# Performance work log

Measured on AMD Instinct MI355X. Metric: run time of the kernel, lower is better.

Reference implementation:

```python
import jax, jax.numpy as jnp
import numpy as np

N = 65536
SIZES = [3, 256, 256, 256, 256, 1]
NU = np.float32(0.01 / np.pi)  # viscosity coefficient 0.01/pi


def setup_inputs() -> dict:
    key = jax.random.key(0)
    ks = jax.random.split(key, 16)
    inp = {
        "t": jax.random.uniform(ks[0], (N, 1), dtype=jnp.float32),
        "x": jax.random.uniform(ks[1], (N, 1), dtype=jnp.float32),
        "y": jax.random.uniform(ks[2], (N, 1), dtype=jnp.float32),
    }
    for i in range(len(SIZES) - 1):
        fan_in, fan_out = SIZES[i], SIZES[i + 1]
        scale = jnp.float32(1.0 / np.sqrt(fan_in))
        inp[f"W{i}"] = jax.random.normal(ks[3 + i], (fan_in, fan_out), dtype=jnp.float32) * scale
        inp[f"b{i}"] = jnp.zeros((fan_out,), dtype=jnp.float32)
    return inp


def reference(t, x, y, W0, b0, W1, b1, W2, b2, W3, b3, W4, b4):
    Ws = (W0, W1, W2, W3, W4)
    bs = (b0, b1, b2, b3, b4)

    def u_scalar(pt):  # pt: (3,) -> scalar u(t,x,y)
        h = pt
        for W, b in zip(Ws[:-1], bs[:-1]):
            h = jnp.tanh(h @ W + b)
        return (h @ Ws[-1] + bs[-1])[0]

    def point(pt):
        u, g = jax.value_and_grad(u_scalar)(pt)          # g = (u_t, u_x, u_y)
        H = jax.jacfwd(jax.grad(u_scalar))(pt)           # 3x3 Hessian (fwd-over-rev)
        f = g[0] + u * g[1] + u * g[2] - NU * (H[1, 1] + H[2, 2])
        return u, f

    pts = jnp.concatenate((t, x, y), axis=1)  # [N, 3]
    u, f = jax.vmap(point)(pts)
    return u[:, None], f[:, None]
```

## Files before the change

### kernel.cpp

```cpp
#include <hip/hip_runtime.h>

#define NPTS 65536
#define NU_F 0.0031830988618379067f

typedef __attribute__((ext_vector_type(8))) _Float16 half8v;
typedef __attribute__((ext_vector_type(2))) __fp16   fp16x2;
typedef __attribute__((ext_vector_type(4))) float    f32x4;

__device__ __forceinline__ unsigned pk2(float a, float b) {
    union { fp16x2 h; unsigned u; } c;
    c.h = __builtin_amdgcn_cvt_pkrtz(a, b);
    return c.u;
}

__device__ __forceinline__ void jet5(float z, float zt, float zx, float zy, float zl,
                                     float& s0, float& s1, float& s2, float& s3, float& s4) {
    float e  = __expf(2.0f * z);
    float a  = 1.0f - 2.0f * __builtin_amdgcn_rcpf(e + 1.0f);
    float ap = 1.0f - a * a;
    s0 = a;
    s1 = ap * zt;
    s2 = ap * zx;
    s3 = ap * zy;
    float q = zx * zx + zy * zy;
    s4 = ap * __builtin_fmaf(-2.0f * a, q, zl);
}

__device__ __forceinline__ int swzoff(int sp, int byteInRow) {
    return (sp << 9) + (byteInRow ^ ((sp & 31) << 4));
}
__device__ __forceinline__ void storeJ2(char* baseB, int sp, int j0,
                                        unsigned lo, unsigned hi) {
    *(uint2*)(baseB + swzoff(sp, j0 * 2)) = make_uint2(lo, hi);
}

__global__ __launch_bounds__(256)
void pinn_prep_kernel(const float* __restrict__ W1, const float* __restrict__ W2,
                      const float* __restrict__ W3, _Float16* __restrict__ ws) {
    int gid  = blockIdx.x * 256 + threadIdx.x;
    int l    = gid >> 13;
    int rem  = gid & 8191;
    int M    = rem >> 9;
    int kt   = (rem >> 6) & 7;
    int lane = rem & 63;
    const float* W = (l == 0) ? W1 : (l == 1) ? W2 : W3;
    int j  = M * 16 + (lane & 15);
    int k0 = kt * 32 + (lane >> 4) * 8;
    union { _Float16 h[8]; half8v v; } hf;
    #pragma unroll
    for (int jj = 0; jj < 8; ++jj)
        hf.h[jj] = (_Float16)W[(k0 + jj) * 256 + j];
    ((half8v*)ws)[l * 8192 + (M * 8 + kt) * 64 + lane] = hf.v;
}

__global__ __launch_bounds__(512, 2)
void pinn_burger2d_kernel(
    const float* __restrict__ t, const float* __restrict__ x, const float* __restrict__ y,
    const float* __restrict__ W0, const float* __restrict__ b0,
    const float* __restrict__ b1, const float* __restrict__ b2, const float* __restrict__ b3,
    const float* __restrict__ W4, const float* __restrict__ b4,
    const _Float16* __restrict__ wf, float* __restrict__ out)
{
    __shared__ _Float16 BjS[5 * 16 * 256];
    char* bjB = (char*)BjS;

    const int tid  = threadIdx.x;
    const int lane = tid & 63;
    const int wv   = tid >> 6;
    const int p    = lane & 15;
    const int quad = lane >> 4;
    const int base = blockIdx.x * 16;
    const int gi   = base + p;

    const float tv = t[gi], xv = x[gi], yv = y[gi];

    #pragma unroll
    for (int m = 0; m < 2; ++m) {
        const int j0 = wv * 32 + m * 16 + quad * 4;
        float4 w0t = *(const float4*)(W0 + j0);
        float4 w0x = *(const float4*)(W0 + 256 + j0);
        float4 w0y = *(const float4*)(W0 + 512 + j0);
        float4 bb  = *(const float4*)(b0 + j0);
        float wtA[4] = {w0t.x, w0t.y, w0t.z, w0t.w};
        float wxA[4] = {w0x.x, w0x.y, w0x.z, w0x.w};
        float wyA[4] = {w0y.x, w0y.y, w0y.z, w0y.w};
        float bbA[4] = {bb.x, bb.y, bb.z, bb.w};
        float ss[5][4];
        #pragma unroll
        for (int i = 0; i < 4; ++i) {
            float z = tv * wtA[i] + xv * wxA[i] + yv * wyA[i] + bbA[i];
            jet5(z, wtA[i], wxA[i], wyA[i], 0.0f,
                 ss[0][i], ss[1][i], ss[2][i], ss[3][i], ss[4][i]);
        }
        #pragma unroll
        for (int s = 0; s < 5; ++s)
            storeJ2(bjB, s * 16 + p, j0, pk2(ss[s][0], ss[s][1]), pk2(ss[s][2], ss[s][3]));
    }
    __syncthreads();

    f32x4 acc[2][5];

    for (int li = 0; li < 3; ++li) {
        #pragma unroll
        for (int m = 0; m < 2; ++m)
            #pragma unroll
            for (int c = 0; c < 5; ++c)
                acc[m][c] = (f32x4)(0.0f);

        const half8v* whf = (const half8v*)wf + li * 8192;

        #pragma unroll 2
        for (int kt = 0; kt < 8; ++kt) {
            const int bRow = kt * 64 + quad * 16;
            half8v bv0 = *(const half8v*)(bjB + swzoff(     p, bRow));
            half8v bv1 = *(const half8v*)(bjB + swzoff(16 + p, bRow));
            half8v bv2 = *(const half8v*)(bjB + swzoff(32 + p, bRow));
            half8v bv3 = *(const half8v*)(bjB + swzoff(48 + p, bRow));
            half8v bv4 = *(const half8v*)(bjB + swzoff(64 + p, bRow));
            __builtin_amdgcn_s_setprio(1);
            #pragma unroll
            for (int m = 0; m < 2; ++m) {
                half8v wh = whf[((wv * 2 + m) * 8 + kt) * 64 + lane];
                acc[m][0] = __builtin_amdgcn_mfma_f32_16x16x32_f16(wh, bv0, acc[m][0], 0, 0, 0);
                acc[m][1] = __builtin_amdgcn_mfma_f32_16x16x32_f16(wh, bv1, acc[m][1], 0, 0, 0);
                acc[m][2] = __builtin_amdgcn_mfma_f32_16x16x32_f16(wh, bv2, acc[m][2], 0, 0, 0);
                acc[m][3] = __builtin_amdgcn_mfma_f32_16x16x32_f16(wh, bv3, acc[m][3], 0, 0, 0);
                acc[m][4] = __builtin_amdgcn_mfma_f32_16x16x32_f16(wh, bv4, acc[m][4], 0, 0, 0);
            }
            __builtin_amdgcn_s_setprio(0);
        }
        __syncthreads();

        if (li < 2) {
            const float* bL = (li == 0) ? b1 : b2;
            #pragma unroll
            for (int m = 0; m < 2; ++m) {
                const int j0 = (wv * 2 + m) * 16 + quad * 4;
                float4 bb = *(const float4*)(bL + j0);
                float bbA[4] = {bb.x, bb.y, bb.z, bb.w};
                float ss[5][4];
                #pragma unroll
                for (int i = 0; i < 4; ++i) {
                    jet5(acc[m][0][i] + bbA[i], acc[m][1][i], acc[m][2][i],
                         acc[m][3][i], acc[m][4][i],
                         ss[0][i], ss[1][i], ss[2][i], ss[3][i], ss[4][i]);
                }
                #pragma unroll
                for (int s = 0; s < 5; ++s)
                    storeJ2(bjB, s * 16 + p, j0, pk2(ss[s][0], ss[s][1]), pk2(ss[s][2], ss[s][3]));
            }
            __syncthreads();
        }
    }

    float part[5] = {0, 0, 0, 0, 0};
    #pragma unroll
    for (int m = 0; m < 2; ++m) {
        const int j0 = (wv * 2 + m) * 16 + quad * 4;
        float4 bb = *(const float4*)(b3 + j0);
        float4 w4 = *(const float4*)(W4 + j0);
        float bbA[4] = {bb.x, bb.y, bb.z, bb.w};
        float w4A[4] = {w4.x, w4.y, w4.z, w4.w};
        #pragma unroll
        for (int i = 0; i < 4; ++i) {
            float s0, s1, s2, s3, s4;
            jet5(acc[m][0][i] + bbA[i], acc[m][1][i], acc[m][2][i],
                 acc[m][3][i], acc[m][4][i], s0, s1, s2, s3, s4);
            part[0] += s0 * w4A[i];
            part[1] += s1 * w4A[i];
            part[2] += s2 * w4A[i];
            part[3] += s3 * w4A[i];
            part[4] += s4 * w4A[i];
        }
    }
    #pragma unroll
    for (int s = 0; s < 5; ++s) {
        part[s] += __shfl_xor(part[s], 16, 64);
        part[s] += __shfl_xor(part[s], 32, 64);
    }

    float* resf = (float*)BjS;
    if (lane < 16) {
        #pragma unroll
        for (int s = 0; s < 5; ++s) resf[(wv * 5 + s) * 16 + p] = part[s];
    }
    __syncthreads();

    if (tid < 16) {
        const int pp = tid;
        const int g  = base + pp;
        float u = b4[0], ut = 0, ux = 0, uy = 0, lap = 0;
        #pragma unroll
        for (int w = 0; w < 8; ++w) {
            u   += resf[(w * 5 + 0) * 16 + pp];
            ut  += resf[(w * 5 + 1) * 16 + pp];
            ux  += resf[(w * 5 + 2) * 16 + pp];
            uy  += resf[(w * 5 + 3) * 16 + pp];
            lap += resf[(w * 5 + 4) * 16 + pp];
        }
        out[g]        = u;
        out[NPTS + g] = ut + u * ux + u * uy - NU_F * lap;
    }
}

extern "C" void kernel_launch(void* const* d_in, const int* in_sizes, int n_in,
                              void* d_out, int out_size, void* d_ws, size_t ws_size,
                              hipStream_t stream) {
    const float* t  = (const float*)d_in[0];
    const float* x  = (const float*)d_in[1];
    const float* y  = (const float*)d_in[2];
    const float* W0 = (const float*)d_in[3];
    const float* b0 = (const float*)d_in[4];
    const float* W1 = (const float*)d_in[5];
    const float* b1 = (const float*)d_in[6];
    const float* W2 = (const float*)d_in[7];
    const float* b2 = (const float*)d_in[8];
    const float* W3 = (const float*)d_in[9];
    const float* b3 = (const float*)d_in[10];
    const float* W4 = (const float*)d_in[11];
    const float* b4 = (const float*)d_in[12];
    float* out = (float*)d_out;

    pinn_prep_kernel<<<96, 256, 0, stream>>>(W1, W2, W3, (_Float16*)d_ws);
    pinn_burger2d_kernel<<<NPTS / 16, 512, 0, stream>>>(
        t, x, y, W0, b0, b1, b2, b3, W4, b4, (const _Float16*)d_ws, out);
}
```

Before: 146.9 us.

## Process two 16-point tiles per block to reuse weight fragments

Each block now handles 32 points as two 16-point tiles with separate LDS activation buffers and accumulator sets. Each weight fragment loaded from global memory feeds MFMAs for both tiles, halving weight traffic per point and doubling independent MFMA chains. In exchange, accumulator registers and LDS per block double (80 KB), which may lower occupancy under the 2-block launch bound and cause spills.

```diff
diff --git a/kernel.cpp b/kernel.cpp
--- a/kernel.cpp
+++ b/kernel.cpp
@@ -61,18 +61,21 @@
     const float* __restrict__ W4, const float* __restrict__ b4,
     const _Float16* __restrict__ wf, float* __restrict__ out)
 {
-    __shared__ _Float16 BjS[5 * 16 * 256];
-    char* bjB = (char*)BjS;
+    __shared__ _Float16 BjS[2][5 * 16 * 256];
+    char* bufA = (char*)BjS[0];
+    char* bufB = (char*)BjS[1];
 
     const int tid  = threadIdx.x;
     const int lane = tid & 63;
     const int wv   = tid >> 6;
     const int p    = lane & 15;
     const int quad = lane >> 4;
-    const int base = blockIdx.x * 16;
-    const int gi   = base + p;
-
-    const float tv = t[gi], xv = x[gi], yv = y[gi];
+    const int base = blockIdx.x * 32;
+    const int giA  = base + p;
+    const int giB  = base + 16 + p;
+
+    const float tvA = t[giA], xvA = x[giA], yvA = y[giA];
+    const float tvB = t[giB], xvB = x[giB], yvB = y[giB];
 
     #pragma unroll
     for (int m = 0; m < 2; ++m) {
@@ -85,49 +88,80 @@
         float wxA[4] = {w0x.x, w0x.y, w0x.z, w0x.w};
         float wyA[4] = {w0y.x, w0y.y, w0y.z, w0y.w};
         float bbA[4] = {bb.x, bb.y, bb.z, bb.w};
-        float ss[5][4];
+        float sA[5][4], sB[5][4];
         #pragma unroll
         for (int i = 0; i < 4; ++i) {
-            float z = tv * wtA[i] + xv * wxA[i] + yv * wyA[i] + bbA[i];
-            jet5(z, wtA[i], wxA[i], wyA[i], 0.0f,
-                 ss[0][i], ss[1][i], ss[2][i], ss[3][i], ss[4][i]);
-        }
-        #pragma unroll
-        for (int s = 0; s < 5; ++s)
-            storeJ2(bjB, s * 16 + p, j0, pk2(ss[s][0], ss[s][1]), pk2(ss[s][2], ss[s][3]));
+            float zA = tvA * wtA[i] + xvA * wxA[i] + yvA * wyA[i] + bbA[i];
+            jet5(zA, wtA[i], wxA[i], wyA[i], 0.0f,
+                 sA[0][i], sA[1][i], sA[2][i], sA[3][i], sA[4][i]);
+            float zB = tvB * wtA[i] + xvB * wxA[i] + yvB * wyA[i] + bbA[i];
+            jet5(zB, wtA[i], wxA[i], wyA[i], 0.0f,
+                 sB[0][i], sB[1][i], sB[2][i], sB[3][i], sB[4][i]);
+        }
+        #pragma unroll
+        for (int s = 0; s < 5; ++s) {
+            storeJ2(bufA, s * 16 + p, j0, pk2(sA[s][0], sA[s][1]), pk2(sA[s][2], sA[s][3]));
+            storeJ2(bufB, s * 16 + p, j0, pk2(sB[s][0], sB[s][1]), pk2(sB[s][2], sB[s][3]));
+        }
     }
     __syncthreads();
 
-    f32x4 acc[2][5];
+    f32x4 accA[2][5], accB[2][5];
 
     for (int li = 0; li < 3; ++li) {
         #pragma unroll
         for (int m = 0; m < 2; ++m)
             #pragma unroll
-            for (int c = 0; c < 5; ++c)
-                acc[m][c] = (f32x4)(0.0f);
+            for (int c = 0; c < 5; ++c) {
+                accA[m][c] = (f32x4)(0.0f);
+                accB[m][c] = (f32x4)(0.0f);
+            }
 
         const half8v* whf = (const half8v*)wf + li * 8192;
 
         #pragma unroll 2
         for (int kt = 0; kt < 8; ++kt) {
             const int bRow = kt * 64 + quad * 16;
-            half8v bv0 = *(const half8v*)(bjB + swzoff(     p, bRow));
-            half8v bv1 = *(const half8v*)(bjB + swzoff(16 + p, bRow));
-            half8v bv2 = *(const half8v*)(bjB + swzoff(32 + p, bRow));
-            half8v bv3 = *(const half8v*)(bjB + swzoff(48 + p, bRow));
-            half8v bv4 = *(const half8v*)(bjB + swzoff(64 + p, bRow));
-            __builtin_amdgcn_s_setprio(1);
-            #pragma unroll
-            for (int m = 0; m < 2; ++m) {
-                half8v wh = whf[((wv * 2 + m) * 8 + kt) * 64 + lane];
-                acc[m][0] = __builtin_amdgcn_mfma_f32_16x16x32_f16(wh, bv0, acc[m][0], 0, 0, 0);
-                acc[m][1] = __builtin_amdgcn_mfma_f32_16x16x32_f16(wh, bv1, acc[m][1], 0, 0, 0);
-                acc[m][2] = __builtin_amdgcn_mfma_f32_16x16x32_f16(wh, bv2, acc[m][2], 0, 0, 0);
-                acc[m][3] = __builtin_amdgcn_mfma_f32_16x16x32_f16(wh, bv3, acc[m][3], 0, 0, 0);
-                acc[m][4] = __builtin_amdgcn_mfma_f32_16x16x32_f16(wh, bv4, acc[m][4], 0, 0, 0);
-            }
-            __builtin_amdgcn_s_setprio(0);
+            half8v wh0 = whf[((wv * 2 + 0) * 8 + kt) * 64 + lane];
+            half8v wh1 = whf[((wv * 2 + 1) * 8 + kt) * 64 + lane];
+            {
+                half8v v0 = *(const half8v*)(bufA + swzoff(     p, bRow));
+                half8v v1 = *(const half8v*)(bufA + swzoff(16 + p, bRow));
+                half8v v2 = *(const half8v*)(bufA + swzoff(32 + p, bRow));
+                half8v v3 = *(const half8v*)(bufA + swzoff(48 + p, bRow));
+                half8v v4 = *(const half8v*)(bufA + swzoff(64 + p, bRow));
+                __builtin_amdgcn_s_setprio(1);
+                accA[0][0] = __builtin_amdgcn_mfma_f32_16x16x32_f16(wh0, v0, accA[0][0], 0, 0, 0);
+                accA[0][1] = __builtin_amdgcn_mfma_f32_16x16x32_f16(wh0, v1, accA[0][1], 0, 0, 0);
+                accA[0][2] = __builtin_amdgcn_mfma_f32_16x16x32_f16(wh0, v2, accA[0][2], 0, 0, 0);
+                accA[0][3] = __builtin_amdgcn_mfma_f32_16x16x32_f16(wh0, v3, accA[0][3], 0, 0, 0);
+                accA[0][4] = __builtin_amdgcn_mfma_f32_16x16x32_f16(wh0, v4, accA[0][4], 0, 0, 0);
+                accA[1][0] = __builtin_amdgcn_mfma_f32_16x16x32_f16(wh1, v0, accA[1][0], 0, 0, 0);
+                accA[1][1] = __builtin_amdgcn_mfma_f32_16x16x32_f16(wh1, v1, accA[1][1], 0, 0, 0);
+                accA[1][2] = __builtin_amdgcn_mfma_f32_16x16x32_f16(wh1, v2, accA[1][2], 0, 0, 0);
+                accA[1][3] = __builtin_amdgcn_mfma_f32_16x16x32_f16(wh1, v3, accA[1][3], 0, 0, 0);
+                accA[1][4] = __builtin_amdgcn_mfma_f32_16x16x32_f16(wh1, v4, accA[1][4], 0, 0, 0);
+                __builtin_amdgcn_s_setprio(0);
+            }
+            {
+                half8v v0 = *(const half8v*)(bufB + swzoff(     p, bRow));
+                half8v v1 = *(const half8v*)(bufB + swzoff(16 + p, bRow));
+                half8v v2 = *(const half8v*)(bufB + swzoff(32 + p, bRow));
+                half8v v3 = *(const half8v*)(bufB + swzoff(48 + p, bRow));
+                half8v v4 = *(const half8v*)(bufB + swzoff(64 + p, bRow));
+                __builtin_amdgcn_s_setprio(1);
+                accB[0][0] = __builtin_amdgcn_mfma_f32_16x16x32_f16(wh0, v0, accB[0][0], 0, 0, 0);
+                accB[0][1] = __builtin_amdgcn_mfma_f32_16x16x32_f16(wh0, v1, accB[0][1], 0, 0, 0);
+                accB[0][2] = __builtin_amdgcn_mfma_f32_16x16x32_f16(wh0, v2, accB[0][2], 0, 0, 0);
+                accB[0][3] = __builtin_amdgcn_mfma_f32_16x16x32_f16(wh0, v3, accB[0][3], 0, 0, 0);
+                accB[0][4] = __builtin_amdgcn_mfma_f32_16x16x32_f16(wh0, v4, accB[0][4], 0, 0, 0);
+                accB[1][0] = __builtin_amdgcn_mfma_f32_16x16x32_f16(wh1, v0, accB[1][0], 0, 0, 0);
+                accB[1][1] = __builtin_amdgcn_mfma_f32_16x16x32_f16(wh1, v1, accB[1][1], 0, 0, 0);
+                accB[1][2] = __builtin_amdgcn_mfma_f32_16x16x32_f16(wh1, v2, accB[1][2], 0, 0, 0);
+                accB[1][3] = __builtin_amdgcn_mfma_f32_16x16x32_f16(wh1, v3, accB[1][3], 0, 0, 0);
+                accB[1][4] = __builtin_amdgcn_mfma_f32_16x16x32_f16(wh1, v4, accB[1][4], 0, 0, 0);
+                __builtin_amdgcn_s_setprio(0);
+            }
         }
         __syncthreads();
 
@@ -138,22 +172,28 @@
                 const int j0 = (wv * 2 + m) * 16 + quad * 4;
                 float4 bb = *(const float4*)(bL + j0);
                 float bbA[4] = {bb.x, bb.y, bb.z, bb.w};
-                float ss[5][4];
+                float sA[5][4], sB[5][4];
                 #pragma unroll
                 for (int i = 0; i < 4; ++i) {
-                    jet5(acc[m][0][i] + bbA[i], acc[m][1][i], acc[m][2][i],
-                         acc[m][3][i], acc[m][4][i],
-                         ss[0][i], ss[1][i], ss[2][i], ss[3][i], ss[4][i]);
+                    jet5(accA[m][0][i] + bbA[i], accA[m][1][i], accA[m][2][i],
+                         accA[m][3][i], accA[m][4][i],
+                         sA[0][i], sA[1][i], sA[2][i], sA[3][i], sA[4][i]);
+                    jet5(accB[m][0][i] + bbA[i], accB[m][1][i], accB[m][2][i],
+                         accB[m][3][i], accB[m][4][i],
+                         sB[0][i], sB[1][i], sB[2][i], sB[3][i], sB[4][i]);
                 }
                 #pragma unroll
-                for (int s = 0; s < 5; ++s)
-                    storeJ2(bjB, s * 16 + p, j0, pk2(ss[s][0], ss[s][1]), pk2(ss[s][2], ss[s][3]));
+                for (int s = 0; s < 5; ++s) {
+                    storeJ2(bufA, s * 16 + p, j0, pk2(sA[s][0], sA[s][1]), pk2(sA[s][2], sA[s][3]));
+                    storeJ2(bufB, s * 16 + p, j0, pk2(sB[s][0], sB[s][1]), pk2(sB[s][2], sB[s][3]));
+                }
             }
             __syncthreads();
         }
     }
 
-    float part[5] = {0, 0, 0, 0, 0};
+    float pA[5] = {0, 0, 0, 0, 0};
+    float pB[5] = {0, 0, 0, 0, 0};
     #pragma unroll
     for (int m = 0; m < 2; ++m) {
         const int j0 = (wv * 2 + m) * 16 + quad * 4;
@@ -164,39 +204,47 @@
         #pragma unroll
         for (int i = 0; i < 4; ++i) {
             float s0, s1, s2, s3, s4;
-            jet5(acc[m][0][i] + bbA[i], acc[m][1][i], acc[m][2][i],
-                 acc[m][3][i], acc[m][4][i], s0, s1, s2, s3, s4);
-            part[0] += s0 * w4A[i];
-            part[1] += s1 * w4A[i];
-            part[2] += s2 * w4A[i];
-            part[3] += s3 * w4A[i];
-            part[4] += s4 * w4A[i];
+            jet5(accA[m][0][i] + bbA[i], accA[m][1][i], accA[m][2][i],
+                 accA[m][3][i], accA[m][4][i], s0, s1, s2, s3, s4);
+            pA[0] += s0 * w4A[i]; pA[1] += s1 * w4A[i]; pA[2] += s2 * w4A[i];
+            pA[3] += s3 * w4A[i]; pA[4] += s4 * w4A[i];
+            jet5(accB[m][0][i] + bbA[i], accB[m][1][i], accB[m][2][i],
+                 accB[m][3][i], accB[m][4][i], s0, s1, s2, s3, s4);
+            pB[0] += s0 * w4A[i]; pB[1] += s1 * w4A[i]; pB[2] += s2 * w4A[i];
+            pB[3] += s3 * w4A[i]; pB[4] += s4 * w4A[i];
         }
     }
     #pragma unroll
     for (int s = 0; s < 5; ++s) {
-        part[s] += __shfl_xor(part[s], 16, 64);
-        part[s] += __shfl_xor(part[s], 32, 64);
+        pA[s] += __shfl_xor(pA[s], 16, 64);
+        pA[s] += __shfl_xor(pA[s], 32, 64);
+        pB[s] += __shfl_xor(pB[s], 16, 64);
+        pB[s] += __shfl_xor(pB[s], 32, 64);
     }
 
     float* resf = (float*)BjS;
     if (lane < 16) {
         #pragma unroll
-        for (int s = 0; s < 5; ++s) resf[(wv * 5 + s) * 16 + p] = part[s];
+        for (int s = 0; s < 5; ++s) {
+            resf[(wv * 5 + s) * 16 + p]       = pA[s];
+            resf[640 + (wv * 5 + s) * 16 + p] = pB[s];
+        }
     }
     __syncthreads();
 
-    if (tid < 16) {
-        const int pp = tid;
-        const int g  = base + pp;
+    if (tid < 32) {
+        const int tile = tid >> 4;
+        const int pp   = tid & 15;
+        const int off  = tile * 640;
+        const int g    = base + tile * 16 + pp;
         float u = b4[0], ut = 0, ux = 0, uy = 0, lap = 0;
         #pragma unroll
         for (int w = 0; w < 8; ++w) {
-            u   += resf[(w * 5 + 0) * 16 + pp];
-            ut  += resf[(w * 5 + 1) * 16 + pp];
-            ux  += resf[(w * 5 + 2) * 16 + pp];
-            uy  += resf[(w * 5 + 3) * 16 + pp];
-            lap += resf[(w * 5 + 4) * 16 + pp];
+            u   += resf[off + (w * 5 + 0) * 16 + pp];
+            ut  += resf[off + (w * 5 + 1) * 16 + pp];
+            ux  += resf[off + (w * 5 + 2) * 16 + pp];
+            uy  += resf[off + (w * 5 + 3) * 16 + pp];
+            lap += resf[off + (w * 5 + 4) * 16 + pp];
         }
         out[g]        = u;
         out[NPTS + g] = ut + u * ux + u * uy - NU_F * lap;
@@ -222,6 +270,6 @@
     float* out = (float*)d_out;
 
     pinn_prep_kernel<<<96, 256, 0, stream>>>(W1, W2, W3, (_Float16*)d_ws);
-    pinn_burger2d_kernel<<<NPTS / 16, 512, 0, stream>>>(
+    pinn_burger2d_kernel<<<NPTS / 32, 512, 0, stream>>>(
         t, x, y, W0, b0, b1, b2, b3, W4, b4, (const _Float16*)d_ws, out);
 }
```

Result: no change. 148.7 us (+1.2%).
